# Kernel tuning notes

Measured on AMD Instinct MI355X. Metric: run time of the kernel, lower is better.

## Reference

```python
import jax, jax.numpy as jnp
import numpy as np
import math

D1 = D2 = D3 = 256
B, S = 2, 384
SCALE = math.sqrt((D1 + D2 + D3) / 3)  # arc_norm scale


def setup_inputs() -> dict:
    key = jax.random.key(0)
    k1, k2, k3, kw = jax.random.split(key, 4)
    matrix_1 = jax.random.normal(k1, (B, S, D1), dtype=jnp.float32)
    matrix_2 = jax.random.normal(k2, (B, S, D2), dtype=jnp.float32)
    matrix_3 = jax.random.normal(k3, (B, S, D3), dtype=jnp.float32)
    # xavier-uniform-like scale for the trilinear tensor parameter
    W = jax.random.normal(kw, (D1, D2, D3), dtype=jnp.float32) * 0.02
    return {"matrix_1": matrix_1, "matrix_2": matrix_2, "matrix_3": matrix_3, "W": W}


def reference(matrix_1, matrix_2, matrix_3, W):
    _, s, _ = matrix_1.shape
    # mode == 'sib': upper-triangular (diag=1) mask over the (j, k) dims
    mask = jnp.triu(jnp.ones((s, s), dtype=bool), k=1)[None, None, :, :]  # [1,1,S,S]
    # Faithful reproduction of the original einsum chain (note: subscripts are
    # exactly as in the torch module, including the independent sum indices).
    v1U = jnp.einsum('bix,pqr->biqr', matrix_1, W)          # [B,S,D2,D3]
    v1Uv2 = jnp.einsum('biqr,bjx->bijr', v1U, matrix_2)      # [B,S,S,D3]
    scores = jnp.einsum('bkx,bijr->bijk', matrix_3, v1Uv2)   # [B,S,S,S]
    scores = jnp.where(mask, scores, 0.0)                    # masked_fill(~mask, 0)
    return scores / SCALE                                    # activation = Passthrough
```

## Files before the change

### kernel.cpp

```cpp
#include <hip/hip_runtime.h>

#define SS 384
#define BB 2
#define DD 256
#define NPART 1024

typedef float f32x4 __attribute__((ext_vector_type(4)));

#define WS_PART 16
#define WS_M1 2048
#define WS_M2 2816
#define WS_M3 3584

__global__ void stage1_kernel(const float* __restrict__ m1,
                              const float* __restrict__ m2,
                              const float* __restrict__ m3,
                              const float* __restrict__ W,
                              float* __restrict__ ws) {
    if (blockIdx.x < NPART) {
        __shared__ float sm[4];
        const f32x4* W4 = (const f32x4*)W;
        const unsigned n4 = (DD * DD * DD) / 4;
        float s = 0.f;
        for (unsigned i = blockIdx.x * blockDim.x + threadIdx.x; i < n4; i += NPART * 256) {
            f32x4 v = W4[i];
            s += (v.x + v.y) + (v.z + v.w);
        }
        #pragma unroll
        for (int off = 32; off; off >>= 1) s += __shfl_down(s, off, 64);
        int lane = threadIdx.x & 63, w = threadIdx.x >> 6;
        if (lane == 0) sm[w] = s;
        __syncthreads();
        if (threadIdx.x == 0) ws[WS_PART + blockIdx.x] = (sm[0] + sm[1]) + (sm[2] + sm[3]);
    } else {
        int wave = (int)(blockIdx.x - NPART) * 4 + (int)(threadIdx.x >> 6);
        int lane = threadIdx.x & 63;
        if (wave >= 3 * BB * SS) return;
        const float* src;
        float* dst;
        if (wave < BB * SS)          { src = m1 + (size_t)wave * DD;                 dst = ws + WS_M1 + wave; }
        else if (wave < 2 * BB * SS) { src = m2 + (size_t)(wave - BB * SS) * DD;     dst = ws + WS_M2 + (wave - BB * SS); }
        else                         { src = m3 + (size_t)(wave - 2 * BB * SS) * DD; dst = ws + WS_M3 + (wave - 2 * BB * SS); }
        f32x4 v = ((const f32x4*)src)[lane];
        float s = (v.x + v.y) + (v.z + v.w);
        #pragma unroll
        for (int off = 32; off; off >>= 1) s += __shfl_down(s, off, 64);
        if (lane == 0) *dst = s;
    }
}

__global__ void __launch_bounds__(384) writer_kernel(const float* __restrict__ ws,
                                                     float* __restrict__ out) {
    __shared__ float sred[8];
    __shared__ float m2l[SS];
    int t  = threadIdx.x;
    int bi = blockIdx.x;
    int b  = bi >= SS ? 1 : 0;

    m2l[t] = ws[WS_M2 + b * SS + t];
    float r1 = ws[WS_M1 + bi];
    int jrow = t / 96;
    int k4   = t - jrow * 96;
    f32x4 f = ((const f32x4*)(ws + WS_M3 + b * SS))[k4];

    const float* p = ws + WS_PART;
    float s = p[t] + p[t + 384] + (t < 256 ? p[t + 768] : 0.f);
    #pragma unroll
    for (int off = 32; off; off >>= 1) s += __shfl_down(s, off, 64);
    int lane = t & 63, w = t >> 6;
    if (lane == 0) sred[w] = s;
    __syncthreads();
    if (t == 0) {
        float tot = ((sred[0] + sred[1]) + (sred[2] + sred[3])) + (sred[4] + sred[5]);
        sred[6] = tot * (1.0f / 16.0f);
    }
    __syncthreads();
    float c1 = r1 * sred[6];

    int k0 = k4 * 4;
    f32x4* dst = (f32x4*)out + (size_t)bi * (SS * SS / 4);
    #pragma unroll 4
    for (int j = jrow; j < SS; j += 4) {
        float cj = c1 * m2l[j];
        f32x4 o;
        o.x = (k0 + 0 > j) ? cj * f.x : 0.f;
        o.y = (k0 + 1 > j) ? cj * f.y : 0.f;
        o.z = (k0 + 2 > j) ? cj * f.z : 0.f;
        o.w = (k0 + 3 > j) ? cj * f.w : 0.f;
        dst[j * 96 + k4] = o;
    }
}

extern "C" void kernel_launch(void* const* d_in, const int* in_sizes, int n_in,
                              void* d_out, int out_size, void* d_ws, size_t ws_size,
                              hipStream_t stream) {
    const float* m1 = (const float*)d_in[0];
    const float* m2 = (const float*)d_in[1];
    const float* m3 = (const float*)d_in[2];
    const float* W  = (const float*)d_in[3];
    float* out = (float*)d_out;
    float* ws  = (float*)d_ws;

    stage1_kernel<<<NPART + 576, 256, 0, stream>>>(m1, m2, m3, W, ws);
    writer_kernel<<<BB * SS, 384, 0, stream>>>(ws, out);
}
```

Baseline: 107.9 us.

## Remap writer so each thread owns one (j,k4) slot across batch rows

```diff
diff --git a/kernel.cpp b/kernel.cpp
--- a/kernel.cpp
+++ b/kernel.cpp
@@ -4,6 +4,7 @@
 #define BB 2
 #define DD 256
 #define NPART 1024
+#define SLAB4 (SS * SS / 4)
 
 typedef float f32x4 __attribute__((ext_vector_type(4)));
 
@@ -49,45 +50,66 @@
     }
 }
 
-__global__ void __launch_bounds__(384) writer_kernel(const float* __restrict__ ws,
+__global__ void __launch_bounds__(256) writer_kernel(const float* __restrict__ ws,
                                                      float* __restrict__ out) {
     __shared__ float sred[8];
-    __shared__ float m2l[SS];
-    int t  = threadIdx.x;
-    int bi = blockIdx.x;
-    int b  = bi >= SS ? 1 : 0;
-
-    m2l[t] = ws[WS_M2 + b * SS + t];
-    float r1 = ws[WS_M1 + bi];
-    int jrow = t / 96;
-    int k4   = t - jrow * 96;
-    f32x4 f = ((const f32x4*)(ws + WS_M3 + b * SS))[k4];
+    __shared__ float c1l[BB * SS];
+    int t = threadIdx.x;
 
     const float* p = ws + WS_PART;
-    float s = p[t] + p[t + 384] + (t < 256 ? p[t + 768] : 0.f);
+    float s = (p[t] + p[t + 256]) + (p[t + 512] + p[t + 768]);
     #pragma unroll
     for (int off = 32; off; off >>= 1) s += __shfl_down(s, off, 64);
     int lane = t & 63, w = t >> 6;
     if (lane == 0) sred[w] = s;
     __syncthreads();
-    if (t == 0) {
-        float tot = ((sred[0] + sred[1]) + (sred[2] + sred[3])) + (sred[4] + sred[5]);
-        sred[6] = tot * (1.0f / 16.0f);
+    if (t == 0) sred[4] = (((sred[0] + sred[1]) + (sred[2] + sred[3]))) * (1.0f / 16.0f);
+    __syncthreads();
+    float wt16 = sred[4];
+
+    c1l[t]       = ws[WS_M1 + t]       * wt16;
+    c1l[t + 256] = ws[WS_M1 + t + 256] * wt16;
+    c1l[t + 512] = ws[WS_M1 + t + 512] * wt16;
+
+    unsigned g     = blockIdx.x * 256u + t;
+    unsigned which = g / SLAB4;
+    unsigned so    = g - which * SLAB4;
+    int j  = (int)(so / 96);
+    int k4 = (int)(so - (unsigned)j * 96);
+    int k0 = k4 * 4;
+
+    f32x4 fa = ((const f32x4*)(ws + WS_M3))[k4];
+    f32x4 fb = ((const f32x4*)(ws + WS_M3 + SS))[k4];
+    f32x4 fm0, fm1;
+    fm0.x = (k0 + 0 > j) ? fa.x : 0.f;
+    fm0.y = (k0 + 1 > j) ? fa.y : 0.f;
+    fm0.z = (k0 + 2 > j) ? fa.z : 0.f;
+    fm0.w = (k0 + 3 > j) ? fa.w : 0.f;
+    fm1.x = (k0 + 0 > j) ? fb.x : 0.f;
+    fm1.y = (k0 + 1 > j) ? fb.y : 0.f;
+    fm1.z = (k0 + 2 > j) ? fb.z : 0.f;
+    fm1.w = (k0 + 3 > j) ? fb.w : 0.f;
+    float m2v0 = ws[WS_M2 + j];
+    float m2v1 = ws[WS_M2 + SS + j];
+    __syncthreads();
+
+    f32x4* dst = (f32x4*)out + so + (size_t)which * SLAB4;
+    int bi = (int)which;
+    #pragma unroll 4
+    for (; bi < SS; bi += 8) {
+        float cj = c1l[bi] * m2v0;
+        f32x4 o;
+        o.x = cj * fm0.x; o.y = cj * fm0.y; o.z = cj * fm0.z; o.w = cj * fm0.w;
+        *dst = o;
+        dst += 8 * SLAB4;
     }
-    __syncthreads();
-    float c1 = r1 * sred[6];
-
-    int k0 = k4 * 4;
-    f32x4* dst = (f32x4*)out + (size_t)bi * (SS * SS / 4);
     #pragma unroll 4
-    for (int j = jrow; j < SS; j += 4) {
-        float cj = c1 * m2l[j];
+    for (; bi < BB * SS; bi += 8) {
+        float cj = c1l[bi] * m2v1;
         f32x4 o;
-        o.x = (k0 + 0 > j) ? cj * f.x : 0.f;
-        o.y = (k0 + 1 > j) ? cj * f.y : 0.f;
-        o.z = (k0 + 2 > j) ? cj * f.z : 0.f;
-        o.w = (k0 + 3 > j) ? cj * f.w : 0.f;
-        dst[j * 96 + k4] = o;
+        o.x = cj * fm1.x; o.y = cj * fm1.y; o.z = cj * fm1.z; o.w = cj * fm1.w;
+        *dst = o;
+        dst += 8 * SLAB4;
     }
 }
 
@@ -102,5 +124,5 @@
     float* ws  = (float*)d_ws;
 
     stage1_kernel<<<NPART + 576, 256, 0, stream>>>(m1, m2, m3, W, ws);
-    writer_kernel<<<BB * SS, 384, 0, stream>>>(ws, out);
+    writer_kernel<<<1152, 256, 0, stream>>>(ws, out);
 }
```

Measured after the change: 103.6 us. -3.9%, faster.
